# Optimization experiments

Measured on AMD Instinct MI355X. Metric: run time of the kernel, lower is better.

Reference implementation:

```python
import jax, jax.numpy as jnp
import numpy as np


def setup_inputs() -> dict:
    key = jax.random.key(0)
    k1, k2, k3, k4 = jax.random.split(key, 4)
    N_NODES, N_RELS, N_TRIPLES, H = 100000, 100000, 300000, 256
    node_states = jax.random.normal(k1, (N_NODES, H), dtype=jnp.float32)
    rel_states = jax.random.normal(k2, (N_RELS, H), dtype=jnp.float32)
    triples = jax.random.randint(k3, (N_TRIPLES, 3), 0, N_NODES, dtype=jnp.int64)
    # nn.Linear(2H, H): weight (H, 2H) in torch; store transposed (2H, H) for x @ W
    W = jax.random.normal(k4, (2 * H, H), dtype=jnp.float32) * (1.0 / np.sqrt(2 * H))
    b = jnp.zeros((H,), dtype=jnp.float32)
    return {"node_states": node_states, "rel_states": rel_states, "triples": triples, "W": W, "b": b}


def reference(node_states, rel_states, triples, W, b):
    # triples columns: (subj_idx, rel_idx, obj_idx)
    subj_idx, rel_idx, obj_idx = triples[:, 0], triples[:, 1], triples[:, 2]
    rel = rel_states[rel_idx]                              # (T, H)
    msg_s2o = node_states[subj_idx] + rel                  # (T, H)
    msg_o2s = node_states[obj_idx] + rel                   # (T, H)
    agg = jnp.zeros_like(node_states)
    agg = agg.at[obj_idx].add(msg_s2o)
    agg = agg.at[subj_idx].add(msg_o2s)
    h = jnp.concatenate([node_states, agg], axis=-1)       # (N, 2H)
    h = h @ W + b                                          # (N, H)
    h = jax.nn.silu(h)
    return node_states + h
```

## Files before the change

kernel.cpp:

```cpp
#include <hip/hip_runtime.h>

#define H 256
typedef unsigned int  uint;
typedef unsigned short ushort;
typedef float  floatx4 __attribute__((ext_vector_type(4)));
typedef short  shortx8 __attribute__((ext_vector_type(8)));

__device__ __forceinline__ ushort bf16rn(float f) {
    uint u = __float_as_uint(f);
    u += 0x7FFF + ((u >> 16) & 1);
    return (ushort)(u >> 16);
}
__device__ __forceinline__ uint pkbf2(float a, float b) {
    return (uint)bf16rn(a) | ((uint)bf16rn(b) << 16);
}
__device__ __forceinline__ float bf2f(uint lo16) {
    return __uint_as_float(lo16 << 16);
}
__device__ __forceinline__ void atomic_pk_bf16(void* addr, uint v) {
    asm volatile("global_atomic_pk_add_bf16 %0, %1, off" :: "v"(addr), "v"(v) : "memory");
}
__device__ __forceinline__ void glds16(const void* g, void* l) {
    __builtin_amdgcn_global_load_lds(
        (__attribute__((address_space(1))) void*)(unsigned long long)(g),
        (__attribute__((address_space(3))) void*)(l), 16, 0, 0);
}

__global__ __launch_bounds__(256) void wt_kernel(const float* __restrict__ W,
                                                 ushort* __restrict__ Wt) {
    __shared__ ushort tile[64][65];
    int k0 = (blockIdx.x >> 2) * 64;
    int n0 = (blockIdx.x & 3) * 64;
    int tx = threadIdx.x & 63, ty = threadIdx.x >> 6;
#pragma unroll
    for (int i = 0; i < 16; ++i) {
        int k = ty + i * 4;
        tile[k][tx] = bf16rn(W[(size_t)(k0 + k) * H + n0 + tx]);
    }
    __syncthreads();
#pragma unroll
    for (int i = 0; i < 16; ++i) {
        int n = ty + i * 4;
        int k = k0 + tx;
        Wt[(size_t)((k >> 5) * 256 + n0 + n) * 32 + (k & 31)] = tile[tx][n];
    }
}

__global__ __launch_bounds__(256) void prep_kernel(const float* __restrict__ ns,
                                                   char* __restrict__ outbase, int M)
{
    int row = blockIdx.x * 2 + (threadIdx.x >> 7);
    if (row >= M) return;
    int t = threadIdx.x & 127;
    float2 v = ((const float2*)ns)[(size_t)row * 128 + t];
    uint* rp = (uint*)(outbase + (size_t)row * 1024);
    rp[t]       = 0u;
    rp[128 + t] = pkbf2(v.x, v.y);
}

__global__ __launch_bounds__(256) void scatter_kernel(
    const float* __restrict__ rs, const int* __restrict__ trip,
    char* __restrict__ outbase, int n_trip)
{
    int t = blockIdx.x * 2 + (threadIdx.x >> 7);
    if (t >= n_trip) return;
    int p = threadIdx.x & 127;
    int s = trip[3 * t + 0];
    int r = trip[3 * t + 1];
    int o = trip[3 * t + 2];
    uint bs = *(const uint*)(outbase + (size_t)s * 1024 + 512 + p * 4);
    uint bo = *(const uint*)(outbase + (size_t)o * 1024 + 512 + p * 4);
    float2 vr = ((const float2*)rs)[(size_t)r * 128 + p];
    uint m_s2o = pkbf2(bf2f(bs & 0xffffu) + vr.x, bf2f(bs >> 16) + vr.y);
    uint m_o2s = pkbf2(bf2f(bo & 0xffffu) + vr.x, bf2f(bo >> 16) + vr.y);
    atomic_pk_bf16(outbase + (size_t)o * 1024 + p * 4, m_s2o);
    atomic_pk_bf16(outbase + (size_t)s * 1024 + p * 4, m_o2s);
}

__global__ __launch_bounds__(512) void gemm_kernel(
    const float* __restrict__ ns, const char* __restrict__ arows,
    const ushort* __restrict__ Wt, const float* __restrict__ bias,
    float* __restrict__ out, int M)
{
    __shared__ __align__(16) ushort As[2][128 * 32];
    __shared__ __align__(16) ushort Bs[2][256 * 32];

    const int tid  = threadIdx.x;
    const int wave = tid >> 6;
    const int lane = tid & 63;
    const int fm = lane & 15, fq = lane >> 4;
    const int wm = wave >> 2, wn = wave & 3;
    const int rowBase = blockIdx.x * 128;

    floatx4 acc[4][4] = {};

    const int am = tid >> 2, akq = tid & 3;
    int arow = rowBase + am; if (arow >= M) arow = M - 1;
    const char* asrc = arows + (size_t)arow * 1024 + akq * 16;
    const char* wtp  = (const char*)Wt;

#define STAGE(kt, buf)                                                        \
    do {                                                                      \
        glds16(asrc + ((512 + (kt) * 64) & 1023), &As[(buf)][tid * 8]);       \
        glds16(wtp + (size_t)(kt) * 16384 + tid * 16, &Bs[(buf)][tid * 8]);   \
        glds16(wtp + (size_t)(kt) * 16384 + 8192 + tid * 16,                  \
               &Bs[(buf)][4096 + tid * 8]);                                   \
    } while (0)

    STAGE(0, 0);
    __syncthreads();

#pragma unroll
    for (int kt = 0; kt < 16; ++kt) {
        const int cur = kt & 1;
        if (kt < 15) STAGE(kt + 1, cur ^ 1);

        shortx8 aF[4], bF[4];
#pragma unroll
        for (int mi = 0; mi < 4; ++mi)
            aF[mi] = *(const shortx8*)&As[cur][(wm * 64 + mi * 16 + fm) * 32 + fq * 8];
#pragma unroll
        for (int ni = 0; ni < 4; ++ni)
            bF[ni] = *(const shortx8*)&Bs[cur][(wn * 64 + ni * 16 + fm) * 32 + fq * 8];
#pragma unroll
        for (int mi = 0; mi < 4; ++mi)
#pragma unroll
            for (int ni = 0; ni < 4; ++ni)
                acc[mi][ni] = __builtin_amdgcn_mfma_f32_16x16x32_bf16(
                    aF[mi], bF[ni], acc[mi][ni], 0, 0, 0);

        __syncthreads();
    }
#undef STAGE

#pragma unroll
    for (int mi = 0; mi < 4; ++mi) {
#pragma unroll
        for (int ni = 0; ni < 4; ++ni) {
            int col = wn * 64 + ni * 16 + fm;
            float bc = bias[col];
#pragma unroll
            for (int r = 0; r < 4; ++r) {
                int row = rowBase + wm * 64 + mi * 16 + fq * 4 + r;
                if (row < M) {
                    float x = acc[mi][ni][r] + bc;
                    float sg = 1.f / (1.f + __expf(-x));
                    out[(size_t)row * H + col] = ns[(size_t)row * H + col] + x * sg;
                }
            }
        }
    }
}

extern "C" void kernel_launch(void* const* d_in, const int* in_sizes, int n_in,
                              void* d_out, int out_size, void* d_ws, size_t ws_size,
                              hipStream_t stream)
{
    const float* ns   = (const float*)d_in[0];
    const float* rs   = (const float*)d_in[1];
    const int*   tp   = (const int*)d_in[2];
    const float* Wm   = (const float*)d_in[3];
    const float* bias = (const float*)d_in[4];
    const int M      = in_sizes[0] / H;
    const int n_trip = in_sizes[2] / 3;
    float*  out = (float*)d_out;
    ushort* Wt  = (ushort*)d_ws;

    prep_kernel<<<dim3((M + 1) / 2), dim3(256), 0, stream>>>(ns, (char*)out, M);
    wt_kernel<<<dim3(32), dim3(256), 0, stream>>>(Wm, Wt);
    scatter_kernel<<<dim3((n_trip + 1) / 2), dim3(256), 0, stream>>>(
        rs, tp, (char*)out, n_trip);
    gemm_kernel<<<dim3((M + 127) / 128), dim3(512), 0, stream>>>(
        ns, (const char*)out, Wt, bias, out, M);
}
```

Before: 583.2 us.

## Replace atomic scatter with bucketed adjacency fill and per-node gather

Replaces the per-element bf16 atomic scatter with a push-to-pull scheme. Triples are bucketed into a per-node adjacency list (up to 64 edges) stored in the unused half of each output row. A gather kernel then sums neighbour and relation states in fp32 and writes the aggregate once. A fixup pass with atomics handles overflow nodes. This removes the heavy feature-wide atomic traffic, at the cost of extra launches, a memset, random reads of neighbour rows, and a serial per-edge loop per node. It also changes the row layout, so the GEMM A-operand offset is swapped.

```diff
diff --git a/kernel.cpp b/kernel.cpp
--- a/kernel.cpp
+++ b/kernel.cpp
@@ -47,15 +47,89 @@
 }
 
 __global__ __launch_bounds__(256) void prep_kernel(const float* __restrict__ ns,
-                                                   char* __restrict__ outbase, int M)
+                                                   char* __restrict__ outbase,
+                                                   int M, int csr)
 {
     int row = blockIdx.x * 2 + (threadIdx.x >> 7);
     if (row >= M) return;
     int t = threadIdx.x & 127;
     float2 v = ((const float2*)ns)[(size_t)row * 128 + t];
     uint* rp = (uint*)(outbase + (size_t)row * 1024);
-    rp[t]       = 0u;
-    rp[128 + t] = pkbf2(v.x, v.y);
+    if (csr) {
+        rp[t] = pkbf2(v.x, v.y);
+    } else {
+        rp[t]       = 0u;
+        rp[128 + t] = pkbf2(v.x, v.y);
+    }
+}
+
+__global__ __launch_bounds__(256) void fill_kernel(const int* __restrict__ trip,
+                                                   char* __restrict__ outbase,
+                                                   uint* __restrict__ cnt,
+                                                   uint* __restrict__ flag, int n_trip)
+{
+    int t = blockIdx.x * 256 + threadIdx.x;
+    if (t >= n_trip) return;
+    int s = trip[3 * t + 0];
+    int r = trip[3 * t + 1];
+    int o = trip[3 * t + 2];
+    uint i0 = atomicAdd(&cnt[o], 1u);
+    if (i0 < 64u) { int2 e; e.x = s; e.y = r;
+        *(int2*)(outbase + (size_t)o * 1024 + 512 + (size_t)i0 * 8) = e; }
+    else atomicExch(flag, 1u);
+    uint i1 = atomicAdd(&cnt[s], 1u);
+    if (i1 < 64u) { int2 e; e.x = o; e.y = r;
+        *(int2*)(outbase + (size_t)s * 1024 + 512 + (size_t)i1 * 8) = e; }
+    else atomicExch(flag, 1u);
+}
+
+__global__ __launch_bounds__(256) void gather_kernel(const float* __restrict__ rs,
+                                                     char* __restrict__ outbase,
+                                                     const uint* __restrict__ cnt, int M)
+{
+    int node = blockIdx.x * 4 + (threadIdx.x >> 6);
+    if (node >= M) return;
+    int l = threadIdx.x & 63;
+    char* row = outbase + (size_t)node * 1024;
+    uint c = cnt[node];
+    float4 acc = {0.f, 0.f, 0.f, 0.f};
+    if (c <= 64u) {
+        for (uint e = 0; e < c; ++e) {
+            int2 ed = *(const int2*)(row + 512 + (size_t)e * 8);
+            uint2 nb = *(const uint2*)(outbase + (size_t)ed.x * 1024 + l * 8);
+            float4 vr = *(const float4*)((const char*)rs + (size_t)ed.y * 1024 + l * 16);
+            acc.x += bf2f(nb.x & 0xffffu) + vr.x;
+            acc.y += bf2f(nb.x >> 16)     + vr.y;
+            acc.z += bf2f(nb.y & 0xffffu) + vr.z;
+            acc.w += bf2f(nb.y >> 16)     + vr.w;
+        }
+    }
+    uint2 o2; o2.x = pkbf2(acc.x, acc.y); o2.y = pkbf2(acc.z, acc.w);
+    *(uint2*)(row + 512 + l * 8) = o2;
+}
+
+__global__ __launch_bounds__(256) void fixup_kernel(
+    const float* __restrict__ rs, const int* __restrict__ trip,
+    char* __restrict__ outbase, const uint* __restrict__ cnt,
+    const uint* __restrict__ flag, int n_trip)
+{
+    if (flag[0] == 0u) return;
+    int t = blockIdx.x * 256 + threadIdx.x;
+    if (t >= n_trip) return;
+    int s = trip[3 * t + 0];
+    int r = trip[3 * t + 1];
+    int o = trip[3 * t + 2];
+#pragma unroll 1
+    for (int pass = 0; pass < 2; ++pass) {
+        int dst = pass ? s : o, oth = pass ? o : s;
+        if (cnt[dst] <= 64u) continue;
+        for (int p = 0; p < 128; ++p) {
+            uint nb = *(const uint*)(outbase + (size_t)oth * 1024 + p * 4);
+            float2 vr = ((const float2*)rs)[(size_t)r * 128 + p];
+            atomic_pk_bf16(outbase + (size_t)dst * 1024 + 512 + p * 4,
+                           pkbf2(bf2f(nb & 0xffffu) + vr.x, bf2f(nb >> 16) + vr.y));
+        }
+    }
 }
 
 __global__ __launch_bounds__(256) void scatter_kernel(
@@ -80,7 +154,7 @@
 __global__ __launch_bounds__(512) void gemm_kernel(
     const float* __restrict__ ns, const char* __restrict__ arows,
     const ushort* __restrict__ Wt, const float* __restrict__ bias,
-    float* __restrict__ out, int M)
+    float* __restrict__ out, int M, int aswap)
 {
     __shared__ __align__(16) ushort As[2][128 * 32];
     __shared__ __align__(16) ushort Bs[2][256 * 32];
@@ -101,7 +175,7 @@
 
 #define STAGE(kt, buf)                                                        \
     do {                                                                      \
-        glds16(asrc + ((512 + (kt) * 64) & 1023), &As[(buf)][tid * 8]);       \
+        glds16(asrc + ((aswap + (kt) * 64) & 1023), &As[(buf)][tid * 8]);     \
         glds16(wtp + (size_t)(kt) * 16384 + tid * 16, &Bs[(buf)][tid * 8]);   \
         glds16(wtp + (size_t)(kt) * 16384 + 8192 + tid * 16,                  \
                &Bs[(buf)][4096 + tid * 8]);                                   \
@@ -166,10 +240,27 @@
     float*  out = (float*)d_out;
     ushort* Wt  = (ushort*)d_ws;
 
-    prep_kernel<<<dim3((M + 1) / 2), dim3(256), 0, stream>>>(ns, (char*)out, M);
-    wt_kernel<<<dim3(32), dim3(256), 0, stream>>>(Wm, Wt);
-    scatter_kernel<<<dim3((n_trip + 1) / 2), dim3(256), 0, stream>>>(
-        rs, tp, (char*)out, n_trip);
-    gemm_kernel<<<dim3((M + 127) / 128), dim3(512), 0, stream>>>(
-        ns, (const char*)out, Wt, bias, out, M);
-}
+    size_t ws_need = 256 * 1024 + (size_t)M * 4 + 4;
+    if (ws_size >= ws_need) {
+        uint* cnt  = (uint*)((char*)d_ws + 256 * 1024);
+        uint* flag = cnt + M;
+        hipMemsetAsync(cnt, 0, (size_t)M * 4 + 4, stream);
+        prep_kernel<<<dim3((M + 1) / 2), dim3(256), 0, stream>>>(ns, (char*)out, M, 1);
+        wt_kernel<<<dim3(32), dim3(256), 0, stream>>>(Wm, Wt);
+        fill_kernel<<<dim3((n_trip + 255) / 256), dim3(256), 0, stream>>>(
+            tp, (char*)out, cnt, flag, n_trip);
+        gather_kernel<<<dim3((M + 3) / 4), dim3(256), 0, stream>>>(
+            rs, (char*)out, cnt, M);
+        fixup_kernel<<<dim3((n_trip + 255) / 256), dim3(256), 0, stream>>>(
+            rs, tp, (char*)out, cnt, flag, n_trip);
+        gemm_kernel<<<dim3((M + 127) / 128), dim3(512), 0, stream>>>(
+            ns, (const char*)out, Wt, bias, out, M, 0);
+    } else {
+        prep_kernel<<<dim3((M + 1) / 2), dim3(256), 0, stream>>>(ns, (char*)out, M, 0);
+        wt_kernel<<<dim3(32), dim3(256), 0, stream>>>(Wm, Wt);
+        scatter_kernel<<<dim3((n_trip + 1) / 2), dim3(256), 0, stream>>>(
+            rs, tp, (char*)out, n_trip);
+        gemm_kernel<<<dim3((M + 127) / 128), dim3(512), 0, stream>>>(
+            ns, (const char*)out, Wt, bias, out, M, 512);
+    }
+}
```

Measured after the change: 514.5 us. 1.13x faster.
